# Performance work log

Measured on AMD Instinct MI355X. Metric: run time of the kernel, lower is better.

## Reference

```python
import jax, jax.numpy as jnp
import numpy as np

B, T, C = 4, 1024, 1024
HEAD_SIZE = 64
H = C // HEAD_SIZE
N_LAYER, LAYER_ID = 24, 12
D_MIX_LORA, D_DECAY_LORA = 32, 64
HEAD_SIZE_DIVISOR = 8
LN_EPS = 1e-5 * HEAD_SIZE_DIVISOR ** 2


def setup_inputs() -> dict:
    key = jax.random.key(0)
    ks = jax.random.split(key, 16)
    x = jax.random.normal(ks[0], (B, T, C), jnp.float32)

    r01 = LAYER_ID / (N_LAYER - 1)          # ratio_0_to_1
    r10 = 1.0 - LAYER_ID / N_LAYER          # ratio_1_to_almost0
    ddd = np.arange(C, dtype=np.float64) / C

    time_maa_x = jnp.asarray((1.0 - ddd ** r10).astype(np.float32))
    time_maa_w = jnp.asarray((1.0 - ddd ** r10).astype(np.float32))
    time_maa_k = jnp.asarray((1.0 - ddd ** r10).astype(np.float32))
    time_maa_v = jnp.asarray((1.0 - (ddd ** r10 + 0.3 * r01)).astype(np.float32))
    time_maa_r = jnp.asarray((1.0 - ddd ** (0.5 * r10)).astype(np.float32))
    time_maa_g = jnp.asarray((1.0 - ddd ** (0.5 * r10)).astype(np.float32))

    n = np.arange(C, dtype=np.float64)
    time_decay = jnp.asarray((-6.0 + 5.0 * (n / (C - 1)) ** (0.7 + 1.3 * r01)).astype(np.float32))
    zigzag = ((n + 1) % 3 - 1) * 0.1
    time_faaaa = jnp.asarray((r01 * (1.0 - n / (C - 1)) + zigzag).astype(np.float32)).reshape(H, HEAD_SIZE)

    u = lambda k, shp: jax.random.uniform(k, shp, jnp.float32, -0.01, 0.01)
    time_maa_w1 = u(ks[1], (C, D_MIX_LORA * 5))   # zeros in orig init; small random for a non-trivial test
    time_maa_w2 = u(ks[2], (5, D_MIX_LORA, C))
    time_decay_w1 = u(ks[3], (C, D_DECAY_LORA))
    time_decay_w2 = u(ks[4], (D_DECAY_LORA, C))

    s = 1.0 / np.sqrt(C)
    Wr = jax.random.normal(ks[5], (C, C), jnp.float32) * s   # stored [in, out]
    Wk = jax.random.normal(ks[6], (C, C), jnp.float32) * s
    Wv = jax.random.normal(ks[7], (C, C), jnp.float32) * s
    Wg = jax.random.normal(ks[8], (C, C), jnp.float32) * s
    Wo = jax.random.normal(ks[9], (C, C), jnp.float32) * s
    ln_w = jnp.ones((C,), jnp.float32)
    ln_b = jnp.zeros((C,), jnp.float32)

    return dict(x=x, time_maa_x=time_maa_x, time_maa_w=time_maa_w, time_maa_k=time_maa_k,
                time_maa_v=time_maa_v, time_maa_r=time_maa_r, time_maa_g=time_maa_g,
                time_maa_w1=time_maa_w1, time_maa_w2=time_maa_w2,
                time_decay=time_decay, time_decay_w1=time_decay_w1, time_decay_w2=time_decay_w2,
                time_faaaa=time_faaaa, Wr=Wr, Wk=Wk, Wv=Wv, Wg=Wg, Wo=Wo, ln_w=ln_w, ln_b=ln_b)


def _wkv6(r, k, v, w, u):
    # r,k,v,w: [B,T,H,N]; u: [H,N]. Data-dependent linear recurrence per head.
    def step(S, inp):               # S: [B,H,N,N] (key dim j, value dim i)
        r_t, k_t, v_t, w_t = inp    # each [B,H,N]
        y = jnp.einsum('bhj,bhji->bhi', r_t, S) \
            + jnp.sum(r_t * u * k_t, axis=-1, keepdims=True) * v_t
        decay = jnp.exp(-jnp.exp(w_t))            # CUDA kernel: w_eff = exp(-exp(w))
        S = decay[..., None] * S + k_t[..., None] * v_t[..., None, :]
        return S, y

    to_t = lambda a: jnp.transpose(a, (1, 0, 2, 3))  # [T,B,H,N]
    S0 = jnp.zeros(r.shape[:1] + (r.shape[2], r.shape[3], r.shape[3]), r.dtype)
    _, ys = jax.lax.scan(step, S0, (to_t(r), to_t(k), to_t(v), to_t(w)))
    return jnp.transpose(ys, (1, 0, 2, 3))            # [B,T,H,N]


def reference(x, time_maa_x, time_maa_w, time_maa_k, time_maa_v, time_maa_r, time_maa_g,
              time_maa_w1, time_maa_w2, time_decay, time_decay_w1, time_decay_w2,
              time_faaaa, Wr, Wk, Wv, Wg, Wo, ln_w, ln_b):
    b, t, c = x.shape
    h, n = H, HEAD_SIZE

    # token shift: ZeroPad2d((0,0,1,-1)) shifts time right by one with zero pad
    xx = jnp.concatenate([jnp.zeros_like(x[:, :1]), x[:, :-1]], axis=1) - x
    xxx = x + xx * time_maa_x
    mix = jnp.tanh(xxx @ time_maa_w1).reshape(b, t, 5, D_MIX_LORA)
    m = jnp.einsum('btsd,sdc->sbtc', mix, time_maa_w2)  # [5,B,T,C]
    xw = x + xx * (time_maa_w + m[0])
    xk = x + xx * (time_maa_k + m[1])
    xv = x + xx * (time_maa_v + m[2])
    xr = x + xx * (time_maa_r + m[3])
    xg = x + xx * (time_maa_g + m[4])

    r = xr @ Wr
    k = xk @ Wk
    v = xv @ Wv
    g = jax.nn.silu(xg @ Wg)
    w = time_decay + jnp.tanh(xw @ time_decay_w1) @ time_decay_w2

    y = _wkv6(r.reshape(b, t, h, n), k.reshape(b, t, h, n),
              v.reshape(b, t, h, n), w.reshape(b, t, h, n), time_faaaa)

    # GroupNorm with n_head groups over channel dim, eps = 1e-5 * divisor^2
    mu = y.mean(-1, keepdims=True)
    var = y.var(-1, keepdims=True)
    yn = ((y - mu) / jnp.sqrt(var + LN_EPS)).reshape(b, t, c) * ln_w + ln_b

    return (yn * g) @ Wo
```

## Files before the change

kernel.cpp:

```cpp
#include <hip/hip_runtime.h>

typedef unsigned short u16;
typedef short short8 __attribute__((ext_vector_type(8)));
typedef short short4v __attribute__((ext_vector_type(4)));
typedef float float4v __attribute__((ext_vector_type(4)));
typedef unsigned uint4v __attribute__((ext_vector_type(4)));

__device__ __forceinline__ float bf2f(u16 h) { return __uint_as_float(((unsigned)h) << 16); }
__device__ __forceinline__ u16 f2bf(float f) {
  unsigned u = __float_as_uint(f);
  unsigned r = (u + 0x7fffu + ((u >> 16) & 1u)) >> 16;
  return (u16)r;
}
__device__ __forceinline__ bool is_f32(const void* probe) {
  return ((const u16*)probe)[0] != 0x3F80;
}
__device__ __forceinline__ float ldin(const void* p, long i, bool f32m) {
  return f32m ? ((const float*)p)[i] : bf2f(((const u16*)p)[i]);
}

typedef __attribute__((address_space(1))) const unsigned int as1_u32;
typedef __attribute__((address_space(3))) unsigned int as3_u32;
__device__ __forceinline__ void gl2lds16(const void* g, void* l) {
  __builtin_amdgcn_global_load_lds((as1_u32*)g, (as3_u32*)l, 16, 0, 0);
}

template <int CTRL>
__device__ __forceinline__ float dpp_add(float x) {
  int s = __builtin_amdgcn_update_dpp(0, __float_as_int(x), CTRL, 0xF, 0xF, true);
  return x + __int_as_float(s);
}

__global__ __launch_bounds__(256) void sentinel_fill(u16* o, long n) {
  long i = (long)blockIdx.x * 256 + threadIdx.x;
  if (i < n) o[i] = 0x42C8;
}

struct TDescArr {
  const void* src[13];
  u16* dst[13];
  int rows[13];
  int cols[13];
  int roff[13];
};

__global__ __launch_bounds__(256) void transpose_all(TDescArr d, const void* probe) {
  bool f32m = is_f32(probe);
  int z = blockIdx.z;
  int rows = d.rows[z], cols = d.cols[z], roff = d.roff[z];
  int bc = blockIdx.x * 32, br = blockIdx.y * 32;
  if (bc >= cols || br >= rows) return;
  const void* src = d.src[z];
  u16* dst = d.dst[z];
  __shared__ u16 tile[32][33];
  int tx = threadIdx.x & 31, ty = threadIdx.x >> 5;
#pragma unroll
  for (int i = 0; i < 32; i += 8)
    tile[ty + i][tx] = f2bf(ldin(src, (long)(roff + br + ty + i) * cols + bc + tx, f32m));
  __syncthreads();
#pragma unroll
  for (int i = 0; i < 32; i += 8)
    dst[(long)(bc + ty + i) * rows + br + tx] = tile[tx][ty + i];
}

__global__ __launch_bounds__(256) void token_shift(const void* __restrict__ x,
                                                   const void* __restrict__ maa_x,
                                                   u16* __restrict__ xxx) {
  bool f32m = is_f32(maa_x);
  long idx = (long)blockIdx.x * 256 + threadIdx.x;
  int c = (int)(idx & 1023);
  int tt = (int)((idx >> 10) & 1023);
  float xv = ldin(x, idx, f32m);
  float xp = tt > 0 ? ldin(x, idx - 1024, f32m) : 0.f;
  xxx[idx] = f2bf(xv + (xp - xv) * ldin(maa_x, c, f32m));
}

template <int EPI>
__device__ __forceinline__ void gemm128_core(const u16* __restrict__ A,
                                             const u16* __restrict__ Bt,
                                             void* __restrict__ Cv, int N, int K,
                                             int m0, int n0, u16* As, u16* Bs,
                                             bool f32m) {
  int t = threadIdx.x, lane = t & 63, w = t >> 6;
  int wm = (w >> 1) * 64, wn = (w & 1) * 64;
  int lr = lane & 15, lk = lane >> 4;
  float4v acc[4][4];
#pragma unroll
  for (int i = 0; i < 4; i++)
#pragma unroll
    for (int j = 0; j < 4; j++) acc[i][j] = (float4v){0.f, 0.f, 0.f, 0.f};
  int srow = t >> 3;
  int scol = ((t & 7) ^ (srow & 7)) * 8;
  const u16* Ag = A + (long)(m0 + srow) * K + scol;
  const u16* Bg = Bt + (long)(n0 + srow) * K + scol;
  int so = w * 512;
  for (int k0 = 0; k0 < K; k0 += 64) {
    __syncthreads();
#pragma unroll
    for (int p = 0; p < 4; p++) {
      gl2lds16(Ag + (long)p * 32 * K + k0, As + p * 2048 + so);
      gl2lds16(Bg + (long)p * 32 * K + k0, Bs + p * 2048 + so);
    }
    __syncthreads();
    short8 af[4][2], bfr[4][2];
#pragma unroll
    for (int i = 0; i < 4; i++) {
      int R = wm + i * 16 + lr;
#pragma unroll
      for (int h = 0; h < 2; h++) {
        int j = h * 4 + lk;
        af[i][h] = *(const short8*)(As + R * 64 + (j ^ (R & 7)) * 8);
      }
    }
#pragma unroll
    for (int i = 0; i < 4; i++) {
      int R = wn + i * 16 + lr;
#pragma unroll
      for (int h = 0; h < 2; h++) {
        int j = h * 4 + lk;
        bfr[i][h] = *(const short8*)(Bs + R * 64 + (j ^ (R & 7)) * 8);
      }
    }
#pragma unroll
    for (int mi2 = 0; mi2 < 4; mi2++)
#pragma unroll
      for (int ni2 = 0; ni2 < 4; ni2++) {
        acc[mi2][ni2] = __builtin_amdgcn_mfma_f32_16x16x32_bf16(
            af[mi2][0], bfr[ni2][0], acc[mi2][ni2], 0, 0, 0);
        acc[mi2][ni2] = __builtin_amdgcn_mfma_f32_16x16x32_bf16(
            af[mi2][1], bfr[ni2][1], acc[mi2][ni2], 0, 0, 0);
      }
  }
#pragma unroll
  for (int mi2 = 0; mi2 < 4; mi2++) {
#pragma unroll
    for (int ni2 = 0; ni2 < 4; ni2++) {
      int col = n0 + wn + ni2 * 16 + lr;
#pragma unroll
      for (int rr = 0; rr < 4; rr++) {
        long row = m0 + wm + mi2 * 16 + lk * 4 + rr;
        float val = acc[mi2][ni2][rr];
        if (EPI == 1) val = val / (1.f + __expf(-val));
        if (EPI == 2 && f32m) ((float*)Cv)[row * N + col] = val;
        else ((u16*)Cv)[row * N + col] = f2bf(val);
      }
    }
  }
}

template <int EPI>
__global__ __launch_bounds__(256, 2) void gemm_big(const u16* __restrict__ A,
                                                   const u16* __restrict__ Bt,
                                                   void* __restrict__ Cv, int M, int N,
                                                   int K, const void* probe) {
  __shared__ alignas(16) u16 As[128 * 64];
  __shared__ alignas(16) u16 Bs[128 * 64];
  int sid = blockIdx.y * gridDim.x + blockIdx.x;
  int per8 = (gridDim.x * gridDim.y) >> 3;
  int L = (sid & 7) * per8 + (sid >> 3);
  int mi = L / gridDim.y, ni = L % gridDim.y;
  bool f32m = (EPI == 2) ? is_f32(probe) : false;
  gemm128_core<EPI>(A, Bt, Cv, N, K, mi * 128, ni * 128, As, Bs, f32m);
}

template <int EPI0, int EPI1>
__global__ __launch_bounds__(256, 2) void gemm_big2(
    const u16* __restrict__ A0, const u16* __restrict__ Bt0, u16* __restrict__ C0,
    const u16* __restrict__ A1, const u16* __restrict__ Bt1, u16* __restrict__ C1,
    int M, int N, int K) {
  __shared__ alignas(16) u16 As[128 * 64];
  __shared__ alignas(16) u16 Bs[128 * 64];
  int z = blockIdx.z;
  int sid = blockIdx.y * gridDim.x + blockIdx.x;
  int per8 = (gridDim.x * gridDim.y) >> 3;
  int L = (sid & 7) * per8 + (sid >> 3);
  int mi = L / gridDim.y, ni = L % gridDim.y;
  if (z == 0)
    gemm128_core<EPI0>(A0, Bt0, C0, N, K, mi * 128, ni * 128, As, Bs, false);
  else
    gemm128_core<EPI1>(A1, Bt1, C1, N, K, mi * 128, ni * 128, As, Bs, false);
}

template <int EPI>
__global__ __launch_bounds__(256) void gemm_wave(const u16* __restrict__ A, int lda,
                                                 const u16* __restrict__ Bt,
                                                 u16* __restrict__ C, int ldc,
                                                 float* dA_, float* dB_, int Ntot,
                                                 int K, const void* aux0,
                                                 const void* probe,
                                                 const void* __restrict__ xin) {
  int t = threadIdx.x, lane = t & 63, w = t >> 6;
  int m0 = blockIdx.x * 64 + w * 16;
  int span = Ntot / gridDim.y;
  int col0 = blockIdx.y * span;
  const u16* Bp = Bt + (long)col0 * K;
  int lr = lane & 15, lk = lane >> 4;
  bool f32m = (EPI >= 2) ? is_f32(probe) : false;
  int nt = span >> 4;
  for (int g0 = 0; g0 < nt; g0 += 4) {
    int gc = (nt - g0 < 4) ? (nt - g0) : 4;
    float4v acc[4];
#pragma unroll
    for (int i = 0; i < 4; i++) acc[i] = (float4v){0.f, 0.f, 0.f, 0.f};
    for (int k0 = 0; k0 < K; k0 += 32) {
      short8 a = *(const short8*)(A + (long)(m0 + lr) * lda + k0 + lk * 8);
      for (int gi = 0; gi < gc; gi++) {
        int n0 = (g0 + gi) * 16;
        short8 b = *(const short8*)(Bp + (long)(n0 + lr) * K + k0 + lk * 8);
        acc[gi] = __builtin_amdgcn_mfma_f32_16x16x32_bf16(a, b, acc[gi], 0, 0, 0);
      }
    }
    for (int gi = 0; gi < gc; gi++) {
      int col = col0 + (g0 + gi) * 16 + lr;
      if (EPI == 3) {
        long r0 = m0 + lk * 4;
        float xv4[4];
#pragma unroll
        for (int rr = 0; rr < 4; rr++)
          xv4[rr] = ldin(xin, (r0 + rr) * 1024 + col, f32m);
        float xpv = ((int)(r0 & 1023) > 0) ? ldin(xin, (r0 - 1) * 1024 + col, f32m) : 0.f;
        float mv = ldin(aux0, col, f32m);
#pragma unroll
        for (int rr = 0; rr < 4; rr++) {
          float xv = xv4[rr];
          float xp = (rr == 0) ? xpv : xv4[rr - 1];
          C[(r0 + rr) * 1024 + col] = f2bf(xv + (xp - xv) * (mv + acc[gi][rr]));
        }
      } else {
#pragma unroll
        for (int rr = 0; rr < 4; rr++) {
          long row = m0 + lk * 4 + rr;
          float val = acc[gi][rr];
          if (EPI == 0) {
            C[row * ldc + col] = f2bf(val);
          } else if (EPI == 1) {
            float vv = fminf(fmaxf(val, -15.f), 15.f);
            float e = __expf(2.f * vv);
            C[row * ldc + col] = f2bf((e - 1.f) / (e + 1.f));
          } else if (EPI == 2) {
            float wv = val + ldin(aux0, col, f32m);
            float ew = __expf(wv);
            if (row < 2048) dA_[row * 1024 + col] = ew;
            else dB_[(row - 2048) * 1024 + col] = ew;
          }
        }
      }
    }
  }
}

__global__ __launch_bounds__(256) void gemm_wave3_pair(
    const u16* __restrict__ A0, const u16* __restrict__ Bt0, u16* __restrict__ C0,
    const void* __restrict__ maa0, const u16* __restrict__ A1,
    const u16* __restrict__ Bt1, u16* __restrict__ C1,
    const void* __restrict__ maa1, const void* probe,
    const void* __restrict__ xin) {
  int z = blockIdx.z;
  const u16* A = z ? A1 : A0;
  const u16* Bt = z ? Bt1 : Bt0;
  u16* C = z ? C1 : C0;
  const void* maa = z ? maa1 : maa0;
  bool f32m = is_f32(probe);
  int t = threadIdx.x, lane = t & 63, w = t >> 6;
  int m0 = blockIdx.x * 64 + w * 16;
  int col0 = blockIdx.y * 32;
  const u16* Bp = Bt + (long)col0 * 32;
  int lr = lane & 15, lk = lane >> 4;
  float4v acc[2];
  acc[0] = (float4v){0.f, 0.f, 0.f, 0.f};
  acc[1] = (float4v){0.f, 0.f, 0.f, 0.f};
  short8 a = *(const short8*)(A + (long)(m0 + lr) * 160 + lk * 8);
#pragma unroll
  for (int gi = 0; gi < 2; gi++) {
    short8 b = *(const short8*)(Bp + (long)(gi * 16 + lr) * 32 + lk * 8);
    acc[gi] = __builtin_amdgcn_mfma_f32_16x16x32_bf16(a, b, acc[gi], 0, 0, 0);
  }
#pragma unroll
  for (int gi = 0; gi < 2; gi++) {
    int col = col0 + gi * 16 + lr;
    long r0 = m0 + lk * 4;
    float xv4[4];
#pragma unroll
    for (int rr = 0; rr < 4; rr++)
      xv4[rr] = ldin(xin, (r0 + rr) * 1024 + col, f32m);
    float xpv = ((int)(r0 & 1023) > 0) ? ldin(xin, (r0 - 1) * 1024 + col, f32m) : 0.f;
    float mv = ldin(maa, col, f32m);
#pragma unroll
    for (int rr = 0; rr < 4; rr++) {
      float xv = xv4[rr];
      float xp = (rr == 0) ? xpv : xv4[rr - 1];
      C[(r0 + rr) * 1024 + col] = f2bf(xv + (xp - xv) * (mv + acc[gi][rr]));
    }
  }
}

__global__ __launch_bounds__(256) void gemm_n64_tanh(const u16* __restrict__ A,
                                                     const u16* __restrict__ Bt,
                                                     u16* __restrict__ C) {
  int t = threadIdx.x, lane = t & 63, w = t >> 6;
  int m0 = blockIdx.x * 16;
  int n0 = w * 16;
  int lr = lane & 15, lk = lane >> 4;
  float4v acc = (float4v){0.f, 0.f, 0.f, 0.f};
  const u16* Ap = A + (long)(m0 + lr) * 1024;
  const u16* Bp = Bt + (long)(n0 + lr) * 1024;
  for (int k0 = 0; k0 < 1024; k0 += 32) {
    short8 a = *(const short8*)(Ap + k0 + lk * 8);
    short8 b = *(const short8*)(Bp + k0 + lk * 8);
    acc = __builtin_amdgcn_mfma_f32_16x16x32_bf16(a, b, acc, 0, 0, 0);
  }
#pragma unroll
  for (int rr = 0; rr < 4; rr++) {
    long row = m0 + lk * 4 + rr;
    float vv = fminf(fmaxf(acc[rr], -15.f), 15.f);
    float e = __expf(2.f * vv);
    C[row * 64 + n0 + lr] = f2bf((e - 1.f) / (e + 1.f));
  }
}

__global__ __launch_bounds__(256) void wkv6_chunk(
    const u16* __restrict__ r, const u16* __restrict__ k, const u16* __restrict__ v,
    const float* __restrict__ ewA, const float* __restrict__ ewB,
    const void* __restrict__ u_, const void* probe, u16* __restrict__ y) {
  bool f32m = is_f32(probe);
  int bx = blockIdx.x;
  int vs = bx >> 6, bh = bx & 63;
  int b = bh >> 4, h = bh & 15;
  int tid = threadIdx.x, lane = tid & 63, w = tid >> 6;
  int lr = lane & 15, lk = lane >> 4;

  __shared__ alignas(16) float sc[32][68];
  __shared__ alignas(16) u16 Rp[32][72];
  __shared__ alignas(16) u16 Kp[32][72];
  __shared__ alignas(16) u16 KdF[64 * 40 + 56];
  __shared__ alignas(16) u16 Vt[32][40];
  __shared__ alignas(16) u16 Pb[32][40];
  __shared__ alignas(16) u16 Sh[32][72];
  __shared__ alignas(16) u16 Sl[32][72];
  __shared__ float diag32[32];

  const long base = ((long)b << 20) + h * 64;
  const float* ewg =
      (b < 2 ? ewA + (long)b * 1048576 : ewB + (long)(b - 2) * 1048576) + h * 64;

  int tt = tid >> 3, kg = tid & 7;
  float u8[8];
#pragma unroll
  for (int i = 0; i < 8; i++) u8[i] = ldin(u_, h * 64 + kg * 8 + i, f32m);

  float4v Sst[2];
  Sst[0] = (float4v){0.f, 0.f, 0.f, 0.f};
  Sst[1] = (float4v){0.f, 0.f, 0.f, 0.f};
  int skey = w * 16 + lk * 4;

  for (int c0 = 0; c0 < 1024; c0 += 32) {
    long grow = (long)(c0 + tt) << 10;
    float4v ewlo = *(const float4v*)(ewg + grow + kg * 8);
    float4v ewhi = *(const float4v*)(ewg + grow + kg * 8 + 4);
    short8 rraw = *(const short8*)(r + base + grow + kg * 8);
    short8 kraw = *(const short8*)(k + base + grow + kg * 8);
    short4v vraw = *(const short4v*)(v + base + grow + vs * 32 + kg * 4);
    __syncthreads();
    *(float4v*)&sc[tt][kg * 8] = ewlo;
    *(float4v*)&sc[tt][kg * 8 + 4] = ewhi;
#pragma unroll
    for (int i = 0; i < 4; i++) Vt[kg * 4 + i][tt] = (u16)vraw[i];
#pragma unroll
    for (int vt = 0; vt < 2; vt++) {
      short4v hi4, lo4;
#pragma unroll
      for (int rr = 0; rr < 4; rr++) {
        u16 hv = f2bf(Sst[vt][rr]);
        hi4[rr] = (short)hv;
        lo4[rr] = (short)f2bf(Sst[vt][rr] - bf2f(hv));
      }
      *(short4v*)&Sh[lr + vt * 16][skey] = hi4;
      *(short4v*)&Sl[lr + vt * 16][skey] = lo4;
    }
    __syncthreads();
    if (tid < 64) {
      float vb[32];
#pragma unroll
      for (int t2 = 0; t2 < 32; t2++) vb[t2] = sc[t2][tid];
      float s = 0.f;
#pragma unroll
      for (int t2 = 0; t2 < 32; t2++) {
        s += vb[t2];
        sc[t2][tid] = s;
      }
    }
    __syncthreads();
    {
      float pd = 0.f;
      short8 rpv, kpv;
#pragma unroll
      for (int i = 0; i < 8; i++) {
        int key = kg * 8 + i;
        float rf = bf2f((u16)rraw[i]);
        float kf = bf2f((u16)kraw[i]);
        float si = sc[tt][key];
        float sx = tt ? sc[tt - 1][key] : 0.f;
        float sE = sc[31][key];
        rpv[i] = (short)f2bf(rf * __expf(-sx));
        kpv[i] = (short)f2bf(kf * __expf(si));
        KdF[key * 40 + ((key >> 3) & 7) * 8 + tt] = f2bf(kf * __expf(si - sE));
        pd = fmaf(rf * u8[i], kf, pd);
      }
      *(short8*)&Rp[tt][kg * 8] = rpv;
      *(short8*)&Kp[tt][kg * 8] = kpv;
      pd = dpp_add<0xB1>(pd);
      pd = dpp_add<0x4E>(pd);
      pd = dpp_add<0x104>(pd);
      if (kg == 0) diag32[tt] = pd;
    }
    __syncthreads();
    {
      int pt = w >> 1, pj = w & 1;
      float4v pacc = (float4v){0.f, 0.f, 0.f, 0.f};
      short8 aP0 = *(const short8*)&Rp[pt * 16 + lr][lk * 8];
      short8 aP1 = *(const short8*)&Rp[pt * 16 + lr][lk * 8 + 32];
      short8 bP0 = *(const short8*)&Kp[pj * 16 + lr][lk * 8];
      short8 bP1 = *(const short8*)&Kp[pj * 16 + lr][lk * 8 + 32];
      pacc = __builtin_amdgcn_mfma_f32_16x16x32_bf16(aP0, bP0, pacc, 0, 0, 0);
      pacc = __builtin_amdgcn_mfma_f32_16x16x32_bf16(aP1, bP1, pacc, 0, 0, 0);
      int jcol = pj * 16 + lr;
#pragma unroll
      for (int rr = 0; rr < 4; rr++) {
        int trow = pt * 16 + lk * 4 + rr;
        float val = (jcol < trow) ? pacc[rr] : (jcol == trow ? diag32[trow] : 0.f);
        Pb[trow][jcol] = f2bf(val);
      }
    }
    __syncthreads();
    {
      int yt = w >> 1, yv = w & 1;
      float4v yacc = (float4v){0.f, 0.f, 0.f, 0.f};
      short8 aY = *(const short8*)&Pb[yt * 16 + lr][lk * 8];
      short8 bY = *(const short8*)&Vt[yv * 16 + lr][lk * 8];
      yacc = __builtin_amdgcn_mfma_f32_16x16x32_bf16(aY, bY, yacc, 0, 0, 0);
      short8 aR0 = *(const short8*)&Rp[yt * 16 + lr][lk * 8];
      short8 aR1 = *(const short8*)&Rp[yt * 16 + lr][lk * 8 + 32];
      short8 bH0 = *(const short8*)&Sh[yv * 16 + lr][lk * 8];
      short8 bH1 = *(const short8*)&Sh[yv * 16 + lr][lk * 8 + 32];
      short8 bL0 = *(const short8*)&Sl[yv * 16 + lr][lk * 8];
      short8 bL1 = *(const short8*)&Sl[yv * 16 + lr][lk * 8 + 32];
      yacc = __builtin_amdgcn_mfma_f32_16x16x32_bf16(aR0, bH0, yacc, 0, 0, 0);
      yacc = __builtin_amdgcn_mfma_f32_16x16x32_bf16(aR1, bH1, yacc, 0, 0, 0);
      yacc = __builtin_amdgcn_mfma_f32_16x16x32_bf16(aR0, bL0, yacc, 0, 0, 0);
      yacc = __builtin_amdgcn_mfma_f32_16x16x32_bf16(aR1, bL1, yacc, 0, 0, 0);
#pragma unroll
      for (int rr = 0; rr < 4; rr++) {
        int trow = yt * 16 + lk * 4 + rr;
        y[base + ((long)(c0 + trow) << 10) + vs * 32 + yv * 16 + lr] = f2bf(yacc[rr]);
      }
      int kr = w * 16 + lr;
      short8 aS = *(const short8*)&KdF[kr * 40 + ((kr >> 3) & 7) * 8 + lk * 8];
      short8 bS0 = *(const short8*)&Vt[lr][lk * 8];
      short8 bS1 = *(const short8*)&Vt[16 + lr][lk * 8];
      float4v sa0 = (float4v){0.f, 0.f, 0.f, 0.f};
      float4v sa1 = (float4v){0.f, 0.f, 0.f, 0.f};
      sa0 = __builtin_amdgcn_mfma_f32_16x16x32_bf16(aS, bS0, sa0, 0, 0, 0);
      sa1 = __builtin_amdgcn_mfma_f32_16x16x32_bf16(aS, bS1, sa1, 0, 0, 0);
#pragma unroll
      for (int rr = 0; rr < 4; rr++) {
        float cl = __expf(-sc[31][skey + rr]);
        Sst[0][rr] = fmaf(Sst[0][rr], cl, sa0[rr]);
        Sst[1][rr] = fmaf(Sst[1][rr], cl, sa1[rr]);
      }
    }
  }
}

__global__ __launch_bounds__(256) void gn_gate(const u16* __restrict__ y,
                                               const u16* __restrict__ g,
                                               const void* __restrict__ lnw,
                                               const void* __restrict__ lnb,
                                               const void* probe,
                                               u16* __restrict__ out) {
  bool f32m = is_f32(probe);
  int gid = blockIdx.x * 4 + (threadIdx.x >> 6);
  int lane = threadIdx.x & 63;
  int h = gid & 15;
  long row = gid >> 4;
  long off = row * 1024 + h * 64 + lane;
  float val = bf2f(y[off]);
  float s = val, sq = val * val;
#pragma unroll
  for (int m = 1; m < 64; m <<= 1) {
    s += __shfl_xor(s, m);
    sq += __shfl_xor(sq, m);
  }
  float mean = s * (1.f / 64.f);
  float var = fmaxf(sq * (1.f / 64.f) - mean * mean, 0.f);
  float inv = rsqrtf(var + 6.4e-4f);
  int c = h * 64 + lane;
  float yn = (val - mean) * inv * ldin(lnw, c, f32m) + ldin(lnb, c, f32m);
  out[off] = f2bf(yn * bf2f(g[off]));
}

extern "C" void kernel_launch(void* const* d_in, const int* in_sizes, int n_in,
                              void* d_out, int out_size, void* d_ws, size_t ws_size,
                              hipStream_t stream) {
  const void* x = d_in[0];
  const void* maaX = d_in[1];
  const void* maa_s[5] = {d_in[2], d_in[3], d_in[4], d_in[5], d_in[6]};
  const void* w1 = d_in[7];
  const void* w2 = d_in[8];
  const void* tdec = d_in[9];
  const void* dw1 = d_in[10];
  const void* dw2 = d_in[11];
  const void* faaaa = d_in[12];
  const void* Wr = d_in[13];
  const void* Wk = d_in[14];
  const void* Wv = d_in[15];
  const void* Wg = d_in[16];
  const void* Wo = d_in[17];
  const void* lnw = d_in[18];
  const void* lnb = d_in[19];

  const long oWoT = 4194304;
  const long ow1T = 5242880;
  const long odw1T = 5406720;
  const long odw2T = 5472256;
  const long ow2T = 5537792;
  const long omixb = 5701632;
  const long owtan = 6356992;
  const long oxxxg = 6619136;
  const long omx = 10813440;
  const long orb = 15007744;
  const long okb = 19202048;
  const long ovb = 23396352;
  const long oyb = 27590656;
  const long oend = 31784960;
  const size_t needed = (size_t)oend * 2;

  if (ws_size < needed) {
    sentinel_fill<<<dim3((unsigned)((out_size + 255) / 256)), 256, 0, stream>>>(
        (u16*)d_out, out_size);
    return;
  }

  u16* W = (u16*)d_ws;
  u16* WrT = W;
  u16* WkT = W + 1048576;
  u16* WvT = W + 2097152;
  u16* WgT = W + 3145728;
  u16* WoT = W + oWoT;
  u16* w1T = W + ow1T;
  u16* dw1T = W + odw1T;
  u16* dw2T = W + odw2T;
  u16* w2T = W + ow2T;
  u16* mixb = W + omixb;
  u16* wtan = W + owtan;
  u16* xxxg = W + oxxxg;
  u16* mx = W + omx;
  u16* rbuf = W + orb;
  u16* kbuf = W + okb;
  u16* vbuf = W + ovb;
  u16* ybuf = W + oyb;
  float* dA_ = (float*)W;
  float* dB_ = (float*)(W + omx);
  u16* gated = mx;

  TDescArr td;
  const void* s5[5] = {Wr, Wk, Wv, Wg, Wo};
  u16* t5[5] = {WrT, WkT, WvT, WgT, WoT};
  for (int i = 0; i < 13; i++) td.roff[i] = 0;
  for (int i = 0; i < 5; i++) {
    td.src[i] = s5[i]; td.dst[i] = t5[i]; td.rows[i] = 1024; td.cols[i] = 1024;
  }
  td.src[5] = w1;  td.dst[5] = w1T;  td.rows[5] = 1024; td.cols[5] = 160;
  td.src[6] = dw1; td.dst[6] = dw1T; td.rows[6] = 1024; td.cols[6] = 64;
  td.src[7] = dw2; td.dst[7] = dw2T; td.rows[7] = 64;   td.cols[7] = 1024;
  for (int s = 0; s < 5; s++) {
    td.src[8 + s] = w2;
    td.dst[8 + s] = w2T + s * 1024 * 32;
    td.rows[8 + s] = 32; td.cols[8 + s] = 1024; td.roff[8 + s] = s * 32;
  }

  transpose_all<<<dim3(32, 32, 13), 256, 0, stream>>>(td, maaX);
  token_shift<<<dim3(16384), 256, 0, stream>>>(x, maaX, xxxg);
  gemm_wave<1><<<dim3(64, 10), 256, 0, stream>>>(xxxg, 1024, w1T, mixb, 160, nullptr,
                                                 nullptr, 160, 1024, nullptr, nullptr,
                                                 nullptr);
  gemm_wave3_pair<<<dim3(64, 32, 2), 256, 0, stream>>>(
      mixb + 3 * 32, w2T + 3 * 32768, mx, maa_s[3],
      mixb + 1 * 32, w2T + 1 * 32768, ybuf, maa_s[1], maaX, x);
  gemm_big2<0, 0><<<dim3(32, 8, 2), 256, 0, stream>>>(mx, WrT, rbuf, ybuf, WkT, kbuf,
                                                      4096, 1024, 1024);
  gemm_wave3_pair<<<dim3(64, 32, 2), 256, 0, stream>>>(
      mixb + 2 * 32, w2T + 2 * 32768, mx, maa_s[2],
      mixb + 4 * 32, w2T + 4 * 32768, ybuf, maa_s[4], maaX, x);
  gemm_big2<0, 1><<<dim3(32, 8, 2), 256, 0, stream>>>(mx, WvT, vbuf, ybuf, WgT, xxxg,
                                                      4096, 1024, 1024);
  gemm_wave<3><<<dim3(64, 32), 256, 0, stream>>>(mixb + 0 * 32, 160, w2T + 0 * 32768,
                                                 mx, 1024, nullptr, nullptr, 1024, 32,
                                                 maa_s[0], maaX, x);
  gemm_n64_tanh<<<dim3(256), 256, 0, stream>>>(mx, dw1T, wtan);
  gemm_wave<2><<<dim3(64, 16), 256, 0, stream>>>(wtan, 64, dw2T, nullptr, 0, dA_, dB_,
                                                 1024, 64, tdec, maaX, nullptr);
  wkv6_chunk<<<dim3(128), 256, 0, stream>>>(rbuf, kbuf, vbuf, dA_, dB_, faaaa, maaX,
                                            ybuf);
  gn_gate<<<dim3(16384), 256, 0, stream>>>(ybuf, xxxg, lnw, lnb, maaX, gated);
  gemm_big<2><<<dim3(32, 8), 256, 0, stream>>>(gated, WoT, d_out, 4096, 1024, 1024, maaX);
}
```

Baseline: 360.8 us.

## Software-pipeline WKV6 chunk loop and parallelize decay prefix sum

Restructures the chunked WKV6 loop so each iteration prefetches the next chunk's r/k/v/decay from global memory while computing the current chunk, with the decay cumulative sums double-buffered in shared memory. The serial 32-step prefix sum done by 64 threads is replaced by an all-thread segmented scan that uses wave shuffles. This cuts barriers per chunk from five to three and hides global load latency. It costs more shared memory and registers, which may lower occupancy.

After: 357.5 us. No clear change (-0.9%).

```diff
diff --git a/kernel.cpp b/kernel.cpp
--- a/kernel.cpp
+++ b/kernel.cpp
@@ -329,7 +329,8 @@
   int tid = threadIdx.x, lane = tid & 63, w = tid >> 6;
   int lr = lane & 15, lk = lane >> 4;
 
-  __shared__ alignas(16) float sc[32][68];
+  __shared__ alignas(16) float raw[32][68];
+  __shared__ alignas(16) float scc[2][32][68];
   __shared__ alignas(16) u16 Rp[32][72];
   __shared__ alignas(16) u16 Kp[32][72];
   __shared__ alignas(16) u16 KdF[64 * 40 + 56];
@@ -344,6 +345,8 @@
       (b < 2 ? ewA + (long)b * 1048576 : ewB + (long)(b - 2) * 1048576) + h * 64;
 
   int tt = tid >> 3, kg = tid & 7;
+  int ck = w * 16 + (lane & 15);
+  int cq = lane >> 4;
   float u8[8];
 #pragma unroll
   for (int i = 0; i < 8; i++) u8[i] = ldin(u_, h * 64 + kg * 8 + i, f32m);
@@ -353,41 +356,32 @@
   Sst[1] = (float4v){0.f, 0.f, 0.f, 0.f};
   int skey = w * 16 + lk * 4;
 
-  for (int c0 = 0; c0 < 1024; c0 += 32) {
-    long grow = (long)(c0 + tt) << 10;
+  {
+    long grow = (long)tt << 10;
     float4v ewlo = *(const float4v*)(ewg + grow + kg * 8);
     float4v ewhi = *(const float4v*)(ewg + grow + kg * 8 + 4);
     short8 rraw = *(const short8*)(r + base + grow + kg * 8);
     short8 kraw = *(const short8*)(k + base + grow + kg * 8);
     short4v vraw = *(const short4v*)(v + base + grow + vs * 32 + kg * 4);
-    __syncthreads();
-    *(float4v*)&sc[tt][kg * 8] = ewlo;
-    *(float4v*)&sc[tt][kg * 8 + 4] = ewhi;
-#pragma unroll
-    for (int i = 0; i < 4; i++) Vt[kg * 4 + i][tt] = (u16)vraw[i];
-#pragma unroll
-    for (int vt = 0; vt < 2; vt++) {
-      short4v hi4, lo4;
-#pragma unroll
-      for (int rr = 0; rr < 4; rr++) {
-        u16 hv = f2bf(Sst[vt][rr]);
-        hi4[rr] = (short)hv;
-        lo4[rr] = (short)f2bf(Sst[vt][rr] - bf2f(hv));
-      }
-      *(short4v*)&Sh[lr + vt * 16][skey] = hi4;
-      *(short4v*)&Sl[lr + vt * 16][skey] = lo4;
-    }
-    __syncthreads();
-    if (tid < 64) {
-      float vb[32];
-#pragma unroll
-      for (int t2 = 0; t2 < 32; t2++) vb[t2] = sc[t2][tid];
+    *(float4v*)&raw[tt][kg * 8] = ewlo;
+    *(float4v*)&raw[tt][kg * 8 + 4] = ewhi;
+    __syncthreads();
+    {
+      float pseg[8];
       float s = 0.f;
 #pragma unroll
-      for (int t2 = 0; t2 < 32; t2++) {
-        s += vb[t2];
-        sc[t2][tid] = s;
-      }
+      for (int j = 0; j < 8; j++) {
+        s += raw[cq * 8 + j][ck];
+        pseg[j] = s;
+      }
+      float tot = pseg[7], x = tot;
+      float up = __shfl_up(x, 16);
+      if (cq >= 1) x += up;
+      up = __shfl_up(x, 32);
+      if (cq >= 2) x += up;
+      float pre = x - tot;
+#pragma unroll
+      for (int j = 0; j < 8; j++) scc[0][cq * 8 + j][ck] = pre + pseg[j];
     }
     __syncthreads();
     {
@@ -398,9 +392,9 @@
         int key = kg * 8 + i;
         float rf = bf2f((u16)rraw[i]);
         float kf = bf2f((u16)kraw[i]);
-        float si = sc[tt][key];
-        float sx = tt ? sc[tt - 1][key] : 0.f;
-        float sE = sc[31][key];
+        float si = scc[0][tt][key];
+        float sx = tt ? scc[0][tt - 1][key] : 0.f;
+        float sE = scc[0][31][key];
         rpv[i] = (short)f2bf(rf * __expf(-sx));
         kpv[i] = (short)f2bf(kf * __expf(si));
         KdF[key * 40 + ((key >> 3) & 7) * 8 + tt] = f2bf(kf * __expf(si - sE));
@@ -413,7 +407,28 @@
       pd = dpp_add<0x104>(pd);
       if (kg == 0) diag32[tt] = pd;
     }
-    __syncthreads();
+#pragma unroll
+    for (int i = 0; i < 4; i++) Vt[kg * 4 + i][tt] = (u16)vraw[i];
+#pragma unroll
+    for (int vt = 0; vt < 2; vt++) {
+      short4v z4 = (short4v){0, 0, 0, 0};
+      *(short4v*)&Sh[lr + vt * 16][skey] = z4;
+      *(short4v*)&Sl[lr + vt * 16][skey] = z4;
+    }
+    __syncthreads();
+  }
+
+  for (int ci = 0; ci < 32; ++ci) {
+    int c0 = ci << 5;
+    int c0n = (ci == 31) ? c0 : c0 + 32;
+    int pc = ci & 1, pn = pc ^ 1;
+    long grow = (long)(c0n + tt) << 10;
+    float4v ewlo = *(const float4v*)(ewg + grow + kg * 8);
+    float4v ewhi = *(const float4v*)(ewg + grow + kg * 8 + 4);
+    short8 rraw = *(const short8*)(r + base + grow + kg * 8);
+    short8 kraw = *(const short8*)(k + base + grow + kg * 8);
+    short4v vraw = *(const short4v*)(v + base + grow + vs * 32 + kg * 4);
+
     {
       int pt = w >> 1, pj = w & 1;
       float4v pacc = (float4v){0.f, 0.f, 0.f, 0.f};
@@ -431,7 +446,27 @@
         Pb[trow][jcol] = f2bf(val);
       }
     }
-    __syncthreads();
+    *(float4v*)&raw[tt][kg * 8] = ewlo;
+    *(float4v*)&raw[tt][kg * 8 + 4] = ewhi;
+    __syncthreads();
+
+    {
+      float pseg[8];
+      float s = 0.f;
+#pragma unroll
+      for (int j = 0; j < 8; j++) {
+        s += raw[cq * 8 + j][ck];
+        pseg[j] = s;
+      }
+      float tot = pseg[7], x = tot;
+      float up = __shfl_up(x, 16);
+      if (cq >= 1) x += up;
+      up = __shfl_up(x, 32);
+      if (cq >= 2) x += up;
+      float pre = x - tot;
+#pragma unroll
+      for (int j = 0; j < 8; j++) scc[pn][cq * 8 + j][ck] = pre + pseg[j];
+    }
     {
       int yt = w >> 1, yv = w & 1;
       float4v yacc = (float4v){0.f, 0.f, 0.f, 0.f};
@@ -463,11 +498,51 @@
       sa1 = __builtin_amdgcn_mfma_f32_16x16x32_bf16(aS, bS1, sa1, 0, 0, 0);
 #pragma unroll
       for (int rr = 0; rr < 4; rr++) {
-        float cl = __expf(-sc[31][skey + rr]);
+        float cl = __expf(-scc[pc][31][skey + rr]);
         Sst[0][rr] = fmaf(Sst[0][rr], cl, sa0[rr]);
         Sst[1][rr] = fmaf(Sst[1][rr], cl, sa1[rr]);
       }
     }
+    __syncthreads();
+
+    {
+      float pd = 0.f;
+      short8 rpv, kpv;
+#pragma unroll
+      for (int i = 0; i < 8; i++) {
+        int key = kg * 8 + i;
+        float rf = bf2f((u16)rraw[i]);
+        float kf = bf2f((u16)kraw[i]);
+        float si = scc[pn][tt][key];
+        float sx = tt ? scc[pn][tt - 1][key] : 0.f;
+        float sE = scc[pn][31][key];
+        rpv[i] = (short)f2bf(rf * __expf(-sx));
+        kpv[i] = (short)f2bf(kf * __expf(si));
+        KdF[key * 40 + ((key >> 3) & 7) * 8 + tt] = f2bf(kf * __expf(si - sE));
+        pd = fmaf(rf * u8[i], kf, pd);
+      }
+      *(short8*)&Rp[tt][kg * 8] = rpv;
+      *(short8*)&Kp[tt][kg * 8] = kpv;
+      pd = dpp_add<0xB1>(pd);
+      pd = dpp_add<0x4E>(pd);
+      pd = dpp_add<0x104>(pd);
+      if (kg == 0) diag32[tt] = pd;
+    }
+#pragma unroll
+    for (int i = 0; i < 4; i++) Vt[kg * 4 + i][tt] = (u16)vraw[i];
+#pragma unroll
+    for (int vt = 0; vt < 2; vt++) {
+      short4v hi4, lo4;
+#pragma unroll
+      for (int rr = 0; rr < 4; rr++) {
+        u16 hv = f2bf(Sst[vt][rr]);
+        hi4[rr] = (short)hv;
+        lo4[rr] = (short)f2bf(Sst[vt][rr] - bf2f(hv));
+      }
+      *(short4v*)&Sh[lr + vt * 16][skey] = hi4;
+      *(short4v*)&Sl[lr + vt * 16][skey] = lo4;
+    }
+    __syncthreads();
   }
 }
 
```
